# Performance work log

Measured on AMD Instinct MI355X. Metric: run time of the kernel, lower is better.

## Reference

```python
import jax, jax.numpy as jnp
import numpy as np

RADIUS = 5
WIN = (RADIUS - 1) * 2 + 1  # 9


def setup_inputs() -> dict:
    key = jax.random.key(0)
    k1, k2 = jax.random.split(key)
    B, K, H, W = 4, 4, 224, 224
    seg = jax.random.uniform(k1, (B, K, H, W), dtype=jnp.float32)
    weight = jax.random.uniform(k2, (B, 1, H, W, WIN, WIN), dtype=jnp.float32)
    return {"seg": seg, "weight": weight}


def reference(seg, weight):
    # seg: [B,K,H,W]; weight: [B,1,H,W,w,w] local affinity window, w = 2*(radius-1)+1
    B, K, H, W = seg.shape
    Kconst = jnp.float32(K)
    # torch pads by `radius` on all sides but only uses window offsets 0..2*(radius-1),
    # i.e. relative offsets [-radius, radius-2] -- replicate exactly.
    padded = jnp.pad(seg, ((0, 0), (0, 0), (RADIUS, RADIUS), (RADIUS, RADIUS)))
    # weighted sum over the local window without materializing [B,K,H,W,w,w]
    sum_w_seg = jnp.zeros_like(seg)
    for m in range(WIN):
        for n in range(WIN):
            sum_w_seg = sum_w_seg + padded[:, :, m:m + H, n:n + W] * weight[:, :, :, :, m, n]
    assocA = jnp.sum(sum_w_seg * seg, axis=(-1, -2))                      # [B,K]
    assocV = jnp.sum(jnp.sum(weight, axis=(-1, -2)) * seg, axis=(-1, -2))  # [B,K]
    assoc = jnp.sum(assocA / assocV, axis=-1)                              # [B]
    return jnp.sum(Kconst - assoc)
```

## Files before the change

kernel.cpp:

```cpp
#include <hip/hip_runtime.h>

#define RADIUS 5
#define WIN 9
#define BB 4
#define KK 4
#define HH 224
#define WW 224
#define HW (HH * WW)
#define PD 234
#define PAREA (PD * PD)
#define NBUCKET 64
#define PARTIAL_FLOATS (NBUCKET * BB * 8)
#define BLOCKS_PER_B (HW / 64)


__global__ __launch_bounds__(256) void ncuts_pad(
    const float* __restrict__ seg, float4* __restrict__ pseg)
{
    const int tid = blockIdx.x * 256 + threadIdx.x;
    if (tid >= BB * PAREA) return;
    const int b  = tid / PAREA;
    const int rc = tid - b * PAREA;
    const int r  = rc / PD;
    const int c  = rc - r * PD;
    const int hh = r - RADIUS;
    const int ww = c - RADIUS;
    float4 v = {0.f, 0.f, 0.f, 0.f};
    if (hh >= 0 && hh < HH && ww >= 0 && ww < WW) {
        const float* sb = seg + (size_t)b * KK * HW + hh * WW + ww;
        v.x = sb[0 * HW];
        v.y = sb[1 * HW];
        v.z = sb[2 * HW];
        v.w = sb[3 * HW];
    }
    pseg[tid] = v;
}

__global__ __launch_bounds__(64) void ncuts_main(
    const float* __restrict__ weight,
    const float4* __restrict__ pseg,
    float* __restrict__ partial)
{
    __shared__ float wlds[64 * 81];

    const int lane = threadIdx.x;
    const int tid  = blockIdx.x * 64 + lane;
    const int b    = tid / HW;
    const int rem  = tid - b * HW;
    const int h    = rem / WW;
    const int w    = rem - h * WW;

    const float4* wsrc = (const float4*)(weight + (size_t)blockIdx.x * (64 * 81));
    float4* wdst = (float4*)wlds;
    #pragma unroll
    for (int j = 0; j < 20; ++j)
        wdst[j * 64 + lane] = wsrc[j * 64 + lane];
    if (lane < 16)
        wdst[1280 + lane] = wsrc[1280 + lane];
    __syncthreads();

    const float4* p4 = pseg + (size_t)b * PAREA;
    const float* wl  = &wlds[lane * 81];

    float a0 = 0.f, a1 = 0.f, a2 = 0.f, a3 = 0.f, wsum = 0.f;

    #pragma unroll
    for (int m = 0; m < WIN; ++m) {
        const int base = (h + m) * PD + w;
        #pragma unroll
        for (int n = 0; n < WIN; ++n) {
            const float wv = wl[m * WIN + n];
            const float4 s = p4[base + n];
            a0 = fmaf(wv, s.x, a0);
            a1 = fmaf(wv, s.y, a1);
            a2 = fmaf(wv, s.z, a2);
            a3 = fmaf(wv, s.w, a3);
            wsum += wv;
        }
    }

    const float4 t = p4[(h + RADIUS) * PD + (w + RADIUS)];

    float vals[8] = { a0 * t.x, a1 * t.y, a2 * t.z, a3 * t.w,
                      wsum * t.x, wsum * t.y, wsum * t.z, wsum * t.w };

    #pragma unroll
    for (int i = 0; i < 8; ++i) {
        float v = vals[i];
        v += __shfl_down(v, 32);
        v += __shfl_down(v, 16);
        v += __shfl_down(v, 8);
        v += __shfl_down(v, 4);
        v += __shfl_down(v, 2);
        v += __shfl_down(v, 1);
        vals[i] = v;
    }

    if (lane == 0) {
        const int bb     = blockIdx.x - b * BLOCKS_PER_B;
        const int bucket = bb & (NBUCKET - 1);
        float* dst = partial + (bucket * BB + b) * 8;
        #pragma unroll
        for (int i = 0; i < 8; ++i)
            atomicAdd(dst + i, vals[i]);
    }
}

__global__ __launch_bounds__(64) void ncuts_final(
    const float* __restrict__ partial, float* __restrict__ out)
{
    __shared__ float sums[32];
    const int t = threadIdx.x;
    if (t < 32) {
        const int b = t >> 3;
        const int i = t & 7;
        float s = 0.f;
        for (int bucket = 0; bucket < NBUCKET; ++bucket)
            s += partial[(bucket * BB + b) * 8 + i];
        sums[b * 8 + i] = s;
    }
    __syncthreads();
    if (t == 0) {
        float total = 0.f;
        for (int b = 0; b < BB; ++b) {
            float assoc = 0.f;
            for (int k = 0; k < KK; ++k) {
                const float A = sums[b * 8 + k];
                const float V = sums[b * 8 + 4 + k];
                assoc += A / V;
            }
            total += (float)KK - assoc;
        }
        out[0] = total;
    }
}

extern "C" void kernel_launch(void* const* d_in, const int* in_sizes, int n_in,
                              void* d_out, int out_size, void* d_ws, size_t ws_size,
                              hipStream_t stream) {
    const float* seg    = (const float*)d_in[0];
    const float* weight = (const float*)d_in[1];
    float* out     = (float*)d_out;
    float* wsf     = (float*)d_ws;
    float* partial = wsf;
    float4* pseg   = (float4*)(wsf + PARTIAL_FLOATS);

    hipMemsetAsync(d_ws, 0, PARTIAL_FLOATS * sizeof(float), stream);

    {
        const int total = BB * PAREA;
        const int grid  = (total + 255) / 256;
        hipLaunchKernelGGL(ncuts_pad, dim3(grid), dim3(256), 0, stream, seg, pseg);
    }

    {
        const int grid = BB * BLOCKS_PER_B;
        hipLaunchKernelGGL(ncuts_main, dim3(grid), dim3(64), 0, stream,
                           weight, pseg, partial);
    }

    hipLaunchKernelGGL(ncuts_final, dim3(1), dim3(64), 0, stream, partial, out);
}
```

Measured before the change: 106.9 us.

## Fuse memset and final reduction into pad/main kernels; use direct global-to-LDS loads

The memset is folded into the pad kernel, which now also zeroes the partial buffer and a counter. The separate final kernel is replaced by a last-block-done pattern in the main kernel: an atomic counter lets the last block sum the buckets and write the output. The weight staging now uses global_load_lds so data goes straight from global memory into LDS without passing through registers, and the centre seg load is hoisted before the barrier. Together these cut two launches and some register traffic, at the cost of an extra fence and atomic in every block.

Measured after the change: 230.1 us. +115.3%, slower.

```diff
diff --git a/kernel.cpp b/kernel.cpp
--- a/kernel.cpp
+++ b/kernel.cpp
@@ -11,13 +11,16 @@
 #define PAREA (PD * PD)
 #define NBUCKET 64
 #define PARTIAL_FLOATS (NBUCKET * BB * 8)
+#define ZERO_FLOATS 2304
 #define BLOCKS_PER_B (HW / 64)
+#define TOTAL_BLOCKS (BB * BLOCKS_PER_B)
 
 
 __global__ __launch_bounds__(256) void ncuts_pad(
-    const float* __restrict__ seg, float4* __restrict__ pseg)
+    const float* __restrict__ seg, float4* __restrict__ pseg, float* __restrict__ zr)
 {
     const int tid = blockIdx.x * 256 + threadIdx.x;
+    if (tid < ZERO_FLOATS) zr[tid] = 0.f;
     if (tid >= BB * PAREA) return;
     const int b  = tid / PAREA;
     const int rc = tid - b * PAREA;
@@ -39,7 +42,9 @@
 __global__ __launch_bounds__(64) void ncuts_main(
     const float* __restrict__ weight,
     const float4* __restrict__ pseg,
-    float* __restrict__ partial)
+    float* __restrict__ partial,
+    unsigned* __restrict__ counter,
+    float* __restrict__ out)
 {
     __shared__ float wlds[64 * 81];
 
@@ -51,16 +56,25 @@
     const int w    = rem - h * WW;
 
     const float4* wsrc = (const float4*)(weight + (size_t)blockIdx.x * (64 * 81));
-    float4* wdst = (float4*)wlds;
+    float4* ldsb = (float4*)wlds;
     #pragma unroll
     for (int j = 0; j < 20; ++j)
-        wdst[j * 64 + lane] = wsrc[j * 64 + lane];
+        __builtin_amdgcn_global_load_lds(
+            (__attribute__((address_space(1))) void*)(wsrc + j * 64 + lane),
+            (__attribute__((address_space(3))) void*)(ldsb + j * 64),
+            16, 0, 0);
     if (lane < 16)
-        wdst[1280 + lane] = wsrc[1280 + lane];
+        __builtin_amdgcn_global_load_lds(
+            (__attribute__((address_space(1))) void*)(wsrc + 1280 + lane),
+            (__attribute__((address_space(3))) void*)(ldsb + 1280),
+            16, 0, 0);
+
+    const float4* p4 = pseg + (size_t)b * PAREA;
+    const float4 t = p4[(h + RADIUS) * PD + (w + RADIUS)];
+
     __syncthreads();
 
-    const float4* p4 = pseg + (size_t)b * PAREA;
-    const float* wl  = &wlds[lane * 81];
+    const float* wl = &wlds[lane * 81];
 
     float a0 = 0.f, a1 = 0.f, a2 = 0.f, a3 = 0.f, wsum = 0.f;
 
@@ -78,8 +92,6 @@
             wsum += wv;
         }
     }
-
-    const float4 t = p4[(h + RADIUS) * PD + (w + RADIUS)];
 
     float vals[8] = { a0 * t.x, a1 * t.y, a2 * t.z, a3 * t.w,
                       wsum * t.x, wsum * t.y, wsum * t.z, wsum * t.w };
@@ -104,34 +116,35 @@
         for (int i = 0; i < 8; ++i)
             atomicAdd(dst + i, vals[i]);
     }
-}
 
-__global__ __launch_bounds__(64) void ncuts_final(
-    const float* __restrict__ partial, float* __restrict__ out)
-{
-    __shared__ float sums[32];
-    const int t = threadIdx.x;
-    if (t < 32) {
-        const int b = t >> 3;
-        const int i = t & 7;
+    __threadfence();
+    unsigned old = 0;
+    if (lane == 0) old = atomicAdd(counter, 1u);
+    old = (unsigned)__shfl((int)old, 0);
+    if (old == TOTAL_BLOCKS - 1) {
+        __threadfence();
         float s = 0.f;
-        for (int bucket = 0; bucket < NBUCKET; ++bucket)
-            s += partial[(bucket * BB + b) * 8 + i];
-        sums[b * 8 + i] = s;
-    }
-    __syncthreads();
-    if (t == 0) {
-        float total = 0.f;
-        for (int b = 0; b < BB; ++b) {
-            float assoc = 0.f;
-            for (int k = 0; k < KK; ++k) {
-                const float A = sums[b * 8 + k];
-                const float V = sums[b * 8 + 4 + k];
-                assoc += A / V;
+        if (lane < 32) {
+            #pragma unroll 8
+            for (int bucket = 0; bucket < NBUCKET; ++bucket)
+                s += __hip_atomic_load(partial + bucket * 32 + lane,
+                                       __ATOMIC_RELAXED, __HIP_MEMORY_SCOPE_AGENT);
+            wlds[lane] = s;
+        }
+        __syncthreads();
+        if (lane == 0) {
+            float total = 0.f;
+            for (int bi = 0; bi < BB; ++bi) {
+                float assoc = 0.f;
+                for (int k = 0; k < KK; ++k) {
+                    const float A = wlds[bi * 8 + k];
+                    const float V = wlds[bi * 8 + 4 + k];
+                    assoc += A / V;
+                }
+                total += (float)KK - assoc;
             }
-            total += (float)KK - assoc;
+            out[0] = total;
         }
-        out[0] = total;
     }
 }
 
@@ -140,24 +153,18 @@
                               hipStream_t stream) {
     const float* seg    = (const float*)d_in[0];
     const float* weight = (const float*)d_in[1];
-    float* out     = (float*)d_out;
-    float* wsf     = (float*)d_ws;
-    float* partial = wsf;
-    float4* pseg   = (float4*)(wsf + PARTIAL_FLOATS);
-
-    hipMemsetAsync(d_ws, 0, PARTIAL_FLOATS * sizeof(float), stream);
+    float* out       = (float*)d_out;
+    float* wsf       = (float*)d_ws;
+    float* partial   = wsf;
+    unsigned* counter = (unsigned*)(wsf + 2048);
+    float4* pseg     = (float4*)(wsf + ZERO_FLOATS);
 
     {
         const int total = BB * PAREA;
         const int grid  = (total + 255) / 256;
-        hipLaunchKernelGGL(ncuts_pad, dim3(grid), dim3(256), 0, stream, seg, pseg);
+        hipLaunchKernelGGL(ncuts_pad, dim3(grid), dim3(256), 0, stream, seg, pseg, wsf);
     }
 
-    {
-        const int grid = BB * BLOCKS_PER_B;
-        hipLaunchKernelGGL(ncuts_main, dim3(grid), dim3(64), 0, stream,
-                           weight, pseg, partial);
-    }
-
-    hipLaunchKernelGGL(ncuts_final, dim3(1), dim3(64), 0, stream, partial, out);
+    hipLaunchKernelGGL(ncuts_main, dim3(TOTAL_BLOCKS), dim3(64), 0, stream,
+                       weight, pseg, partial, counter, out);
 }
```
